# Optimization experiments

Hardware: AMD Instinct MI355X
Metric: run time of the kernel (lower is better)

## Reference

```python
import jax, jax.numpy as jnp
from jax import lax
import numpy as np

NUM_LABELS = 15
LABEL_TO_ID = {"O": 0, "B-PERSON": 1, "I-PERSON": 2, "B-LOCATION": 3, "I-LOCATION": 4,
               "B-ORGANIZATION": 5, "I-ORGANIZATION": 6, "B-PHONE": 7, "I-PHONE": 8,
               "B-EMAIL": 9, "I-EMAIL": 10, "B-ID_NUMBER": 11, "I-ID_NUMBER": 12,
               "B-ADDRESS": 13, "I-ADDRESS": 14}


def _pii_constraints():
    """Replicates EnhancedPIICRF._setup_transition_constraints."""
    forbidden = -10000.0
    c = np.zeros((NUM_LABELS, NUM_LABELS), dtype=np.float32)
    pii_types = ['PERSON', 'LOCATION', 'ORGANIZATION', 'PHONE', 'EMAIL', 'ID_NUMBER', 'ADDRESS']
    for t in pii_types:
        b_idx = LABEL_TO_ID[f'B-{t}']
        i_idx = LABEL_TO_ID[f'I-{t}']
        for o in pii_types:
            if o != t:
                c[LABEL_TO_ID[f'B-{o}'], i_idx] = forbidden
        if t in ['PHONE', 'EMAIL', 'ID_NUMBER']:
            c[i_idx, i_idx] = -1.0
    return jnp.asarray(c)


def setup_inputs() -> dict:
    key = jax.random.key(0)
    k1, k2, k3, k4, k5 = jax.random.split(key, 5)
    B, T, L = 512, 4096, NUM_LABELS
    emissions = jax.random.normal(k1, (B, T, L), dtype=jnp.float32)
    labels = jax.random.randint(k2, (B, T), 0, L, dtype=jnp.int64)
    mask = jnp.ones((B, T), dtype=jnp.bool_)
    # torchcrf init: uniform(-0.1, 0.1); constraints added to transitions
    transitions = jax.random.uniform(k3, (L, L), jnp.float32, -0.1, 0.1) + _pii_constraints()
    start_transitions = jax.random.uniform(k4, (L,), jnp.float32, -0.1, 0.1)
    end_transitions = jax.random.uniform(k5, (L,), jnp.float32, -0.1, 0.1)
    return {"emissions": emissions, "transitions": transitions,
            "start_transitions": start_transitions, "end_transitions": end_transitions,
            "labels": labels, "mask": mask}


def reference(emissions, transitions, start_transitions, end_transitions, labels, mask):
    """loss = -mean log-likelihood (torchcrf reduction='mean')."""
    B, T, L = emissions.shape
    maskf = mask.astype(emissions.dtype)
    labels = labels.astype(jnp.int32)

    # ---- numerator: score of the gold path (fully vectorized) ----
    em_score = jnp.take_along_axis(emissions, labels[..., None], axis=2)[..., 0]  # [B,T]
    em_score = (em_score * maskf).sum(axis=1)
    trans_score = (transitions[labels[:, :-1], labels[:, 1:]] * maskf[:, 1:]).sum(axis=1)
    seq_ends = mask.sum(axis=1).astype(jnp.int32) - 1
    last_tags = labels[jnp.arange(B), seq_ends]
    numerator = (start_transitions[labels[:, 0]] + em_score + trans_score
                 + end_transitions[last_tags])

    # ---- denominator: forward algorithm (log-sum-exp recurrence) ----
    alpha0 = start_transitions[None, :] + emissions[:, 0]  # [B,L]

    def step(alpha, xs):
        em_t, m_t = xs  # [B,L], [B]
        nxt = jax.nn.logsumexp(alpha[:, :, None] + transitions[None], axis=1) + em_t
        return jnp.where(m_t[:, None], nxt, alpha), None

    em_T = jnp.swapaxes(emissions, 0, 1)[1:]   # [T-1,B,L]
    mk_T = jnp.swapaxes(mask, 0, 1)[1:]        # [T-1,B]
    alpha, _ = lax.scan(step, alpha0, (em_T, mk_T))
    denominator = jax.nn.logsumexp(alpha + end_transitions[None, :], axis=1)

    llh = numerator - denominator
    return -jnp.mean(llh)
```

## Files before the change

kernel.cpp:

```cpp
#include <hip/hip_runtime.h>


typedef __attribute__((ext_vector_type(8))) __bf16 bf16x8;
typedef __attribute__((ext_vector_type(8))) float f32x8;
typedef __attribute__((ext_vector_type(4))) float f32x4;
typedef __attribute__((ext_vector_type(4))) int   i32x4;
typedef __attribute__((ext_vector_type(2))) float f32x2;

#define BATCH 512
#define TLEN  4096
#define NCH   16
#define CLEN  256
#define LOG2E 1.44269504088896340736f
#define LN2   0.69314718055994530942f

#define SB() __builtin_amdgcn_sched_barrier(0)

__device__ __forceinline__ int pack_bf16_pair(float lo, float hi){
  return __builtin_amdgcn_perm(__float_as_uint(hi), __float_as_uint(lo), 0x07060302);
}

__global__ __launch_bounds__(256, 8) void crf_chunk_kernel(
    const float* __restrict__ em, const float* __restrict__ trans,
    const int* __restrict__ labels,
    float* __restrict__ wsM, float* __restrict__ wsS, float* __restrict__ wsNum)
{
  const int tid   = threadIdx.x;
  const int lane  = tid & 63;
  const int col   = lane & 15;
  const int g     = lane >> 4;
  const int wid   = blockIdx.x * 4 + (tid >> 6);
  const int b     = wid >> 4;
  const int c     = wid & (NCH - 1);
  const int t0    = 1 + c * CLEN;
  const int colc  = (col < 15) ? col : 14;
  const long bT   = (long)b * TLEN;

  const float* emb = em + (bT + t0) * 15 + colc;

  f32x8 e0, e1, e2, e3;

#define LOADE(buf, rr) { const float* _p = emb + (rr) * 120;            \
    buf[0] = _p[0];   buf[1] = _p[15];  buf[2] = _p[30];  buf[3] = _p[45]; \
    buf[4] = _p[60];  buf[5] = _p[75];  buf[6] = _p[90];  buf[7] = _p[105]; }

#define LOADE7(buf) { const float* _p = emb + 31 * 120;                 \
    buf[0] = _p[0];   buf[1] = _p[15];  buf[2] = _p[30];  buf[3] = _p[45]; \
    buf[4] = _p[60];  buf[5] = _p[75];  buf[6] = _p[90]; }

  LOADE(e0, 0);
  LOADE(e1, 1);
  SB();

  {
    const int tA = c * CLEN + lane * 4;
    const int4 lv = *reinterpret_cast<const int4*>(labels + bT + tA);
    const int lpm1 = __shfl(lv.w, lane - 1);
    const float* emA = em + (bT + tA) * 15;
    float a = 0.f;
    float a0 = emA[lv.x] + trans[lpm1 * 15 + lv.x];
    if (lane > 0) a += a0;
    a += emA[15 + lv.y] + trans[lv.x * 15 + lv.y];
    a += emA[30 + lv.z] + trans[lv.y * 15 + lv.z];
    a += emA[45 + lv.w] + trans[lv.z * 15 + lv.w];
    if (lane == 63 && c < NCH - 1){
      const int te = (c + 1) * CLEN;
      const int le = labels[bT + te];
      a += em[(bT + te) * 15 + le] + trans[lv.w * 15 + le];
    }
    #pragma unroll
    for (int off = 1; off < 64; off <<= 1) a += __shfl_xor(a, off);
    if (lane == 0) wsNum[wid] = a;
  }

  f32x2 wa01, wa23;
  {
    float wv[4];
    #pragma unroll
    for (int j = 0; j < 4; ++j){
      const int row = 4 * g + j;
      wv[j] = (row < 15 && col < 15)
            ? __builtin_amdgcn_exp2f(trans[row * 15 + col] * LOG2E) : 0.f;
    }
    wa01[0] = wv[0]; wa01[1] = wv[1]; wa23[0] = wv[2]; wa23[1] = wv[3];
  }

  f32x4 d;
  #pragma unroll
  for (int r = 0; r < 4; ++r) d[r] = (4 * g + r == col) ? 1.f : 0.f;

  const f32x4 zero4 = {0.f, 0.f, 0.f, 0.f};
  int Ki = 0;

#define STEP1(XV) {                                                     \
    const float _E = __builtin_amdgcn_exp2f(XV);                        \
    const f32x2 _e01 = wa01 * _E, _e23 = wa23 * _E;                     \
    i32x4 _ai; _ai[0] = pack_bf16_pair(_e01[0], _e01[1]);               \
               _ai[1] = pack_bf16_pair(_e23[0], _e23[1]);               \
               _ai[2] = 0; _ai[3] = 0;                                  \
    i32x4 _bi; _bi[0] = pack_bf16_pair(d[0], d[1]);                     \
               _bi[1] = pack_bf16_pair(d[2], d[3]);                     \
               _bi[2] = 0; _bi[3] = 0;                                  \
    d = __builtin_amdgcn_mfma_f32_16x16x32_bf16(                        \
          __builtin_bit_cast(bf16x8, _ai), __builtin_bit_cast(bf16x8, _bi), \
          zero4, 0, 0, 0); }

#define BODY8(EB, RN) {                                                 \
    float _add = 0.f;                                                   \
    if (RN) { const int _bits =                                         \
                __builtin_amdgcn_readfirstlane(__float_as_int(d[0]));   \
              const int _K = ((_bits >> 23) & 0xff) - 127;              \
              Ki += _K; _add = (float)(-_K); }                          \
    STEP1(__builtin_fmaf(EB[0], LOG2E, _add));                          \
    STEP1(EB[1] * LOG2E); STEP1(EB[2] * LOG2E); STEP1(EB[3] * LOG2E);   \
    STEP1(EB[4] * LOG2E); STEP1(EB[5] * LOG2E); STEP1(EB[6] * LOG2E);   \
    STEP1(EB[7] * LOG2E); }

#define BODY7(EB) {                                                     \
    const int _bits = __builtin_amdgcn_readfirstlane(__float_as_int(d[0])); \
    const int _K = ((_bits >> 23) & 0xff) - 127;                        \
    Ki += _K; const float _add = (float)(-_K);                          \
    STEP1(__builtin_fmaf(EB[0], LOG2E, _add));                          \
    STEP1(EB[1] * LOG2E); STEP1(EB[2] * LOG2E); STEP1(EB[3] * LOG2E);   \
    STEP1(EB[4] * LOG2E); STEP1(EB[5] * LOG2E); STEP1(EB[6] * LOG2E); }

  if (c != NCH - 1){
    #pragma unroll 1
    for (int rr = 0; rr < 8; ++rr){
      LOADE(e2, 4 * rr + 2); SB(); BODY8(e0, rr != 0);
      LOADE(e3, 4 * rr + 3); SB(); BODY8(e1, 1);
      LOADE(e0, 4 * rr + 4); SB(); BODY8(e2, 1);
      LOADE(e1, 4 * rr + 5); SB(); BODY8(e3, 1);
    }
  } else {
    #pragma unroll 1
    for (int rr = 0; rr < 7; ++rr){
      LOADE(e2, 4 * rr + 2); SB(); BODY8(e0, rr != 0);
      LOADE(e3, 4 * rr + 3); SB(); BODY8(e1, 1);
      LOADE(e0, 4 * rr + 4); SB(); BODY8(e2, 1);
      LOADE(e1, 4 * rr + 5); SB(); BODY8(e3, 1);
    }
    LOADE(e2, 30); SB(); BODY8(e0, 1);
    LOADE7(e3);    SB(); BODY8(e1, 1);
    BODY8(e2, 1);
    BODY7(e3);
  }

#undef LOADE
#undef LOADE7
#undef STEP1
#undef BODY8
#undef BODY7

  *reinterpret_cast<f32x4*>(wsM + (long)wid * 256 + lane * 4) = d;
  if (lane == 0) wsS[wid] = (float)Ki;
}

__global__ __launch_bounds__(64) void crf_combine_kernel(
    const float* __restrict__ em, const float* __restrict__ startT,
    const float* __restrict__ endT, const int* __restrict__ labels,
    const float* __restrict__ wsM, const float* __restrict__ wsS,
    const float* __restrict__ wsNum, float* __restrict__ out)
{
  const int lane = threadIdx.x;
  const int b = blockIdx.x;
  const int n = lane & 15;
  const int nc = (n < 15) ? n : 0;
  const long bT = (long)b * TLEN;

  const float* mp = wsM + (long)(b * NCH) * 256 + lane * 4;
  const float* sp = wsS + b * NCH;
#define LDM(c) *reinterpret_cast<const f32x4*>(mp + (c) * 256)
  f32x4 M0 = LDM(0),  M1 = LDM(1),  M2 = LDM(2),  M3 = LDM(3);
  f32x4 M4 = LDM(4),  M5 = LDM(5),  M6 = LDM(6),  M7 = LDM(7);
  f32x4 M8 = LDM(8),  M9 = LDM(9),  M10 = LDM(10), M11 = LDM(11);
  f32x4 M12 = LDM(12), M13 = LDM(13), M14 = LDM(14), M15 = LDM(15);
#undef LDM
  const float S0 = sp[0],  S1 = sp[1],  S2 = sp[2],  S3 = sp[3];
  const float S4 = sp[4],  S5 = sp[5],  S6 = sp[6],  S7 = sp[7];
  const float S8 = sp[8],  S9 = sp[9],  S10 = sp[10], S11 = sp[11];
  const float S12 = sp[12], S13 = sp[13], S14 = sp[14], S15 = sp[15];

  float v = (n < 15)
          ? __builtin_amdgcn_exp2f((startT[nc] + em[bT * 15 + nc]) * LOG2E) : 0.f;
  float ST = 0.f;

  float np = wsNum[b * NCH + n];
  #pragma unroll
  for (int off = 1; off < 16; off <<= 1) np += __shfl_xor(np, off);

  const int srcl = 16 * (n >> 2) + n;

#define CITER(MC, SC) {                                                 \
    float p0 = MC[0] * v, p1 = MC[1] * v, p2 = MC[2] * v, p3 = MC[3] * v; \
    _Pragma("unroll")                                                   \
    for (int off = 1; off < 16; off <<= 1){   \
      p0 += __shfl_xor(p0, off); p1 += __shfl_xor(p1, off);             \
      p2 += __shfl_xor(p2, off); p3 += __shfl_xor(p3, off);             \
    }                                                                   \
    const float ysel = (n & 2) ? ((n & 1) ? p3 : p2) : ((n & 1) ? p1 : p0); \
    v = __shfl(ysel, srcl);                   \
    ST += SC;                                     \
    float mx = v;                                                       \
    _Pragma("unroll")                                                   \
    for (int off = 1; off < 16; off <<= 1) mx = fmaxf(mx, __shfl_xor(mx, off)); \
    v *= __builtin_amdgcn_rcpf(mx);                                     \
    ST += __builtin_amdgcn_logf(mx); }

  CITER(M0, S0);   CITER(M1, S1);   CITER(M2, S2);   CITER(M3, S3);
  CITER(M4, S4);   CITER(M5, S5);   CITER(M6, S6);   CITER(M7, S7);
  CITER(M8, S8);   CITER(M9, S9);   CITER(M10, S10); CITER(M11, S11);
  CITER(M12, S12); CITER(M13, S13); CITER(M14, S14); CITER(M15, S15);
#undef CITER

  float w = (n < 15) ? v * __builtin_amdgcn_exp2f(endT[nc] * LOG2E) : 0.f;
  #pragma unroll
  for (int off = 1; off < 16; off <<= 1) w += __shfl_xor(w, off);

  if (lane == 0){
    const float den = (__builtin_amdgcn_logf(w) + ST) * LN2;
    const int l0 = labels[bT];
    const int lT = labels[bT + TLEN - 1];
    const float num = np + startT[l0] + em[bT * 15 + l0] + endT[lT];
    atomicAdd(out, (den - num) * (1.0f / BATCH));
  }
}

extern "C" void kernel_launch(void* const* d_in, const int* in_sizes, int n_in,
                              void* d_out, int out_size, void* d_ws, size_t ws_size,
                              hipStream_t stream)
{
  const float* em     = (const float*)d_in[0];
  const float* trans  = (const float*)d_in[1];
  const float* startT = (const float*)d_in[2];
  const float* endT   = (const float*)d_in[3];
  const int*   labels = (const int*)d_in[4];
  float* out = (float*)d_out;

  float* wsNum = (float*)d_ws;
  float* wsS   = (float*)((char*)d_ws + 32768);
  float* wsM   = (float*)((char*)d_ws + 65536);

  hipMemsetAsync(d_out, 0, sizeof(float), stream);

  crf_chunk_kernel<<<BATCH * NCH / 4, 256, 0, stream>>>(em, trans, labels, wsM, wsS, wsNum);
  crf_combine_kernel<<<BATCH, 64, 0, stream>>>(em, startT, endT, labels, wsM, wsS, wsNum, out);
}
```

Before: 267.2 us.

## Stage emissions through LDS with async global_load_lds ring buffer

Replaces the per-lane strided scalar global loads of emissions with contiguous 16-byte global_load_lds transfers into a 4-slot per-wave LDS ring buffer, then reads the values back from LDS for the serial MFMA recurrence. Explicit vmcnt waits keep three loads in flight ahead of consumption. The aim is coalesced, deeper-prefetched memory traffic that hides latency behind the serial chain. In exchange it adds 16 KB of LDS per block, which may limit occupancy, plus extra LDS reads in the critical path.

```diff
diff --git a/kernel.cpp b/kernel.cpp
--- a/kernel.cpp
+++ b/kernel.cpp
@@ -2,7 +2,6 @@
 
 
 typedef __attribute__((ext_vector_type(8))) __bf16 bf16x8;
-typedef __attribute__((ext_vector_type(8))) float f32x8;
 typedef __attribute__((ext_vector_type(4))) float f32x4;
 typedef __attribute__((ext_vector_type(4))) int   i32x4;
 typedef __attribute__((ext_vector_type(2))) float f32x2;
@@ -13,8 +12,6 @@
 #define CLEN  256
 #define LOG2E 1.44269504088896340736f
 #define LN2   0.69314718055994530942f
-
-#define SB() __builtin_amdgcn_sched_barrier(0)
 
 __device__ __forceinline__ int pack_bf16_pair(float lo, float hi){
   return __builtin_amdgcn_perm(__float_as_uint(hi), __float_as_uint(lo), 0x07060302);
@@ -36,21 +33,21 @@
   const int colc  = (col < 15) ? col : 14;
   const long bT   = (long)b * TLEN;
 
-  const float* emb = em + (bT + t0) * 15 + colc;
-
-  f32x8 e0, e1, e2, e3;
-
-#define LOADE(buf, rr) { const float* _p = emb + (rr) * 120;            \
-    buf[0] = _p[0];   buf[1] = _p[15];  buf[2] = _p[30];  buf[3] = _p[45]; \
-    buf[4] = _p[60];  buf[5] = _p[75];  buf[6] = _p[90];  buf[7] = _p[105]; }
-
-#define LOADE7(buf) { const float* _p = emb + 31 * 120;                 \
-    buf[0] = _p[0];   buf[1] = _p[15];  buf[2] = _p[30];  buf[3] = _p[45]; \
-    buf[4] = _p[60];  buf[5] = _p[75];  buf[6] = _p[90]; }
-
-  LOADE(e0, 0);
-  LOADE(e1, 1);
-  SB();
+  __shared__ __align__(16) float lds4[4096];
+  float* lw  = lds4 + (tid >> 6) * 1024;
+  char*  lwb = (char*)lw;
+
+  const long embase = (bT + t0) * 60L;
+  const char* gbase = (const char*)em + (embase - 12);
+  const char* gsrc  = gbase + 16 * (lane < 60 ? lane : 60);
+
+#define GLDS(GP, LOFF) __builtin_amdgcn_global_load_lds(                \
+    (const __attribute__((address_space(1))) void*)(GP),                \
+    (__attribute__((address_space(3))) void*)(lwb + (LOFF)), 16, 0, 0)
+#define STAGE(P) GLDS(gsrc + (P) * 960, ((P) & 3) * 1024)
+
+#define WCNT(n) { asm volatile("s_waitcnt vmcnt(" #n ")" ::: "memory"); \
+                  __builtin_amdgcn_sched_barrier(0); }
 
   {
     const int tA = c * CLEN + lane * 4;
@@ -105,52 +102,82 @@
           __builtin_bit_cast(bf16x8, _ai), __builtin_bit_cast(bf16x8, _bi), \
           zero4, 0, 0, 0); }
 
-#define BODY8(EB, RN) {                                                 \
+#define BODY8(X0,X1,X2,X3,X4,X5,X6,X7, RN) {                            \
     float _add = 0.f;                                                   \
     if (RN) { const int _bits =                                         \
                 __builtin_amdgcn_readfirstlane(__float_as_int(d[0]));   \
               const int _K = ((_bits >> 23) & 0xff) - 127;              \
               Ki += _K; _add = (float)(-_K); }                          \
-    STEP1(__builtin_fmaf(EB[0], LOG2E, _add));                          \
-    STEP1(EB[1] * LOG2E); STEP1(EB[2] * LOG2E); STEP1(EB[3] * LOG2E);   \
-    STEP1(EB[4] * LOG2E); STEP1(EB[5] * LOG2E); STEP1(EB[6] * LOG2E);   \
-    STEP1(EB[7] * LOG2E); }
-
-#define BODY7(EB) {                                                     \
+    STEP1(__builtin_fmaf(X0, LOG2E, _add));                             \
+    STEP1(X1 * LOG2E); STEP1(X2 * LOG2E); STEP1(X3 * LOG2E);            \
+    STEP1(X4 * LOG2E); STEP1(X5 * LOG2E); STEP1(X6 * LOG2E);            \
+    STEP1(X7 * LOG2E); }
+
+#define BODY7(X0,X1,X2,X3,X4,X5,X6) {                                   \
     const int _bits = __builtin_amdgcn_readfirstlane(__float_as_int(d[0])); \
     const int _K = ((_bits >> 23) & 0xff) - 127;                        \
     Ki += _K; const float _add = (float)(-_K);                          \
-    STEP1(__builtin_fmaf(EB[0], LOG2E, _add));                          \
-    STEP1(EB[1] * LOG2E); STEP1(EB[2] * LOG2E); STEP1(EB[3] * LOG2E);   \
-    STEP1(EB[4] * LOG2E); STEP1(EB[5] * LOG2E); STEP1(EB[6] * LOG2E); }
+    STEP1(__builtin_fmaf(X0, LOG2E, _add));                             \
+    STEP1(X1 * LOG2E); STEP1(X2 * LOG2E); STEP1(X3 * LOG2E);            \
+    STEP1(X4 * LOG2E); STEP1(X5 * LOG2E); STEP1(X6 * LOG2E); }
+
+#define CONSUME(P, RN0) {                                               \
+    const float* _lp = lw + ((P) & 3) * 256 + colc;                     \
+    float x0,x1,x2,x3,x4,x5,x6,x7;                                      \
+    x0=_lp[3];   x1=_lp[18];  x2=_lp[33];  x3=_lp[48];                  \
+    x4=_lp[63];  x5=_lp[78];  x6=_lp[93];  x7=_lp[108];                 \
+    BODY8(x0,x1,x2,x3,x4,x5,x6,x7, RN0);                                \
+    x0=_lp[123]; x1=_lp[138]; x2=_lp[153]; x3=_lp[168];                 \
+    x4=_lp[183]; x5=_lp[198]; x6=_lp[213]; x7=_lp[228];                 \
+    BODY8(x0,x1,x2,x3,x4,x5,x6,x7, 1); }
+
+  STAGE(0); STAGE(1); STAGE(2);
 
   if (c != NCH - 1){
     #pragma unroll 1
-    for (int rr = 0; rr < 8; ++rr){
-      LOADE(e2, 4 * rr + 2); SB(); BODY8(e0, rr != 0);
-      LOADE(e3, 4 * rr + 3); SB(); BODY8(e1, 1);
-      LOADE(e0, 4 * rr + 4); SB(); BODY8(e2, 1);
-      LOADE(e1, 4 * rr + 5); SB(); BODY8(e3, 1);
-    }
+    for (int p = 0; p < 13; ++p){
+      STAGE(p + 3);
+      WCNT(3);
+      CONSUME(p, p != 0);
+    }
+    WCNT(2); CONSUME(13, 1);
+    WCNT(1); CONSUME(14, 1);
+    WCNT(0); CONSUME(15, 1);
   } else {
     #pragma unroll 1
-    for (int rr = 0; rr < 7; ++rr){
-      LOADE(e2, 4 * rr + 2); SB(); BODY8(e0, rr != 0);
-      LOADE(e3, 4 * rr + 3); SB(); BODY8(e1, 1);
-      LOADE(e0, 4 * rr + 4); SB(); BODY8(e2, 1);
-      LOADE(e1, 4 * rr + 5); SB(); BODY8(e3, 1);
-    }
-    LOADE(e2, 30); SB(); BODY8(e0, 1);
-    LOADE7(e3);    SB(); BODY8(e1, 1);
-    BODY8(e2, 1);
-    BODY7(e3);
-  }
-
-#undef LOADE
-#undef LOADE7
+    for (int p = 0; p < 12; ++p){
+      STAGE(p + 3);
+      WCNT(3);
+      CONSUME(p, p != 0);
+    }
+    {
+      const char* gsrc56 = gbase + 16 * (lane < 56 ? lane : 56);
+      GLDS(gsrc56 + 15 * 960, (15 & 3) * 1024);
+    }
+    WCNT(3); CONSUME(12, 1);
+    WCNT(2); CONSUME(13, 1);
+    WCNT(1); CONSUME(14, 1);
+    WCNT(0);
+    {
+      const float* _lp = lw + 3 * 256 + colc;
+      float x0,x1,x2,x3,x4,x5,x6,x7;
+      x0=_lp[3];   x1=_lp[18];  x2=_lp[33];  x3=_lp[48];
+      x4=_lp[63];  x5=_lp[78];  x6=_lp[93];  x7=_lp[108];
+      BODY8(x0,x1,x2,x3,x4,x5,x6,x7, 1);
+      float y0,y1,y2,y3,y4,y5,y6;
+      y0=_lp[123]; y1=_lp[138]; y2=_lp[153]; y3=_lp[168];
+      y4=_lp[183]; y5=_lp[198]; y6=_lp[213];
+      BODY7(y0,y1,y2,y3,y4,y5,y6);
+    }
+  }
+
+#undef GLDS
+#undef STAGE
+#undef WCNT
 #undef STEP1
 #undef BODY8
 #undef BODY7
+#undef CONSUME
 
   *reinterpret_cast<f32x4*>(wsM + (long)wid * 256 + lane * 4) = d;
   if (lane == 0) wsS[wid] = (float)Ki;
```

After: 265.5 us. Within noise of the previous version (-0.7%).
